# Performance work log

Hardware: AMD Instinct MI355X
Metric: run time of the kernel (lower is better)

## Reference

```python
import jax, jax.numpy as jnp
import numpy as np

N = 32768      # total nodes
E = 262144     # total edges (avg degree 8)
S = 128        # graph segments
B = 16         # batch entries
C = S // B     # segments per batch entry
NF, NC = 90, 36
OP, OD = 120, 64
D0, DX, GIN, GH = 190, 380, 256, 512


def setup_inputs() -> dict:
    key = jax.random.key(0)
    ks = jax.random.split(key, 16)
    rn = lambda k, shape, s=0.02: jax.random.normal(k, shape, jnp.float32) * s
    return {
        "node_features": jax.random.normal(ks[0], (N, NF), jnp.float32),
        "node_config_features": jax.random.normal(ks[1], (N, NC), jnp.float32),
        "emb_table": rn(ks[2], (OP, OD), 1.0),
        "w1": rn(ks[3], (DX, D0)), "b1": jnp.zeros((DX,), jnp.float32),
        "g1": jnp.ones((DX,), jnp.float32), "be1": jnp.zeros((DX,), jnp.float32),
        "w2": rn(ks[4], (GIN, DX)), "b2": jnp.zeros((GIN,), jnp.float32),
        "g2": jnp.ones((GIN,), jnp.float32), "be2": jnp.zeros((GIN,), jnp.float32),
        "wl1": rn(ks[5], (GH, GIN)), "bl1": jnp.zeros((GH,), jnp.float32), "wr1": rn(ks[6], (GH, GIN)),
        "wl2": rn(ks[7], (GH, GH)), "bl2": jnp.zeros((GH,), jnp.float32), "wr2": rn(ks[8], (GH, GH)),
        "wl3": rn(ks[9], (GH, GH)), "bl3": jnp.zeros((GH,), jnp.float32), "wr3": rn(ks[10], (GH, GH)),
        "wc": rn(ks[11], (1, GH)), "bc": jnp.zeros((1,), jnp.float32),
        "node_ops": jax.random.randint(ks[12], (N,), 0, OP),
        "edges": jax.random.randint(ks[13], (2, E), 0, N),
        # cumulative end indices, equal-size segments; batches = segment -> batch entry
        "node_separation": (jnp.arange(S, dtype=jnp.int32) + 1) * (N // S),
        "batches": jnp.repeat(jnp.arange(B, dtype=jnp.int32), C),
    }


def _leaky(x):
    return jnp.where(x >= 0, x, 0.01 * x)


def _graphwise_ln(x, seg_id, counts, gamma, beta):
    # per-graph-segment mean/var over all nodes and features, per-feature affine
    D = x.shape[1]
    s = jax.ops.segment_sum(jnp.sum(x, -1), seg_id, num_segments=S)
    ss = jax.ops.segment_sum(jnp.sum(x * x, -1), seg_id, num_segments=S)
    cnt = counts.astype(x.dtype) * D
    mean = s / cnt
    var = ss / cnt - mean * mean
    inv = jax.lax.rsqrt(var + 1e-5)
    return (x - mean[seg_id, None]) * inv[seg_id, None] * gamma + beta


def _pairnorm(x):
    # PyG PairNorm, scale=1: center over nodes, divide by sqrt(mean row norm^2)
    xc = x - jnp.mean(x, axis=0, keepdims=True)
    denom = 1e-5 + jnp.sqrt(jnp.mean(jnp.sum(xc * xc, -1)))
    return xc / denom


def _sage(x, src, dst, inv_deg, wl, bl, wr):
    # SAGEConv(mean): lin_l(mean_neighbors) + lin_r(x)
    agg = jax.ops.segment_sum(x[src], dst, num_segments=N) * inv_deg[:, None]
    return agg @ wl.T + bl + x @ wr.T


def reference(node_features, node_config_features, emb_table, w1, b1, g1, be1,
              w2, b2, g2, be2, wl1, bl1, wr1, wl2, bl2, wr2, wl3, bl3, wr3,
              wc, bc, node_ops, edges, node_separation, batches):
    seg_id = jnp.searchsorted(node_separation, jnp.arange(N), side="right")
    counts = jnp.diff(node_separation, prepend=0)
    src, dst = edges[0], edges[1]
    deg = jax.ops.segment_sum(jnp.ones((E,), jnp.float32), dst, num_segments=N)
    inv_deg = 1.0 / jnp.maximum(deg, 1.0)

    x = jnp.concatenate([node_features, node_config_features, emb_table[node_ops]], axis=1)
    # node_features_mlp: Linear -> LeakyReLU -> GLN -> Linear -> LeakyReLU -> GLN
    x = _graphwise_ln(_leaky(x @ w1.T + b1), seg_id, counts, g1, be1)
    x = _graphwise_ln(_leaky(x @ w2.T + b2), seg_id, counts, g2, be2)
    # GraphSAGE: 3 layers, PairNorm + ReLU after all but the last
    x = jax.nn.relu(_pairnorm(_sage(x, src, dst, inv_deg, wl1, bl1, wr1)))
    x = jax.nn.relu(_pairnorm(_sage(x, src, dst, inv_deg, wl2, bl2, wr2)))
    x = _sage(x, src, dst, inv_deg, wl3, bl3, wr3)
    # ragged per-segment sum pooling (replaces the python loop) -> [S, GH]
    seg_sums = jax.ops.segment_sum(x, seg_id, num_segments=S)
    # batches = repeat(arange(B), C) and segments are in order -> reshape groups
    agg = seg_sums.reshape(B, C, GH)
    out = agg @ wc.T + bc  # [B, C, 1]
    return jnp.squeeze(out, 2)
```

## Files before the change

### kernel.cpp

```cpp
#include <hip/hip_runtime.h>
#include <hip/hip_bf16.h>

#define NN   32768
#define EE   262144
#define SS   128
#define NF_  90
#define NC_  36
#define OD_  64
#define D0_  190
#define DX_  380
#define GIN_ 256
#define GH_  512

typedef __attribute__((ext_vector_type(8))) short  s8v;
typedef __attribute__((ext_vector_type(4))) float  f4v;

typedef const __attribute__((address_space(1))) void* gas_ptr;
typedef __attribute__((address_space(3))) void*       las_ptr;

__device__ __forceinline__ float bf2f(unsigned short u) {
  return __uint_as_float(((unsigned)u) << 16);
}
__device__ __forceinline__ unsigned short f2bf(float f) {
  unsigned u = __float_as_uint(f);
  u += 0x7FFFu + ((u >> 16) & 1u);
  return (unsigned short)(u >> 16);
}

__global__ void deg_count(const int* __restrict__ dst, int* __restrict__ deg) {
  int e = blockIdx.x * 256 + threadIdx.x;
  if (e < EE) atomicAdd(&deg[dst[e]], 1);
}

__global__ void inv_deg_k(const int* __restrict__ deg, float* __restrict__ inv_deg) {
  int n = blockIdx.x * 256 + threadIdx.x;
  if (n < NN) inv_deg[n] = 1.0f / fmaxf((float)deg[n], 1.0f);
}

__global__ __launch_bounds__(256) void blk_sum_k(const int* __restrict__ deg,
                                                 int* __restrict__ bsum) {
  __shared__ int buf[256];
  int tid = threadIdx.x;
  buf[tid] = deg[blockIdx.x * 256 + tid];
  __syncthreads();
  for (int off = 128; off > 0; off >>= 1) {
    if (tid < off) buf[tid] += buf[tid + off];
    __syncthreads();
  }
  if (tid == 0) bsum[blockIdx.x] = buf[0];
}

__global__ __launch_bounds__(128) void blk_scan_k(const int* __restrict__ bsum,
                                                  int* __restrict__ boff) {
  __shared__ int buf[128];
  int tid = threadIdx.x;
  int v = bsum[tid];
  buf[tid] = v;
  __syncthreads();
  for (int d = 1; d < 128; d <<= 1) {
    int t = (tid >= d) ? buf[tid - d] : 0;
    __syncthreads();
    if (tid >= d) buf[tid] += t;
    __syncthreads();
  }
  boff[tid] = buf[tid] - v;
}

__global__ __launch_bounds__(256) void offsets_k(const int* __restrict__ deg,
                                                 const int* __restrict__ boff,
                                                 int* __restrict__ offsets) {
  __shared__ int buf[256];
  int tid = threadIdx.x;
  int i = blockIdx.x * 256 + tid;
  int v = deg[i];
  buf[tid] = v;
  __syncthreads();
  for (int d = 1; d < 256; d <<= 1) {
    int t = (tid >= d) ? buf[tid - d] : 0;
    __syncthreads();
    if (tid >= d) buf[tid] += t;
    __syncthreads();
  }
  offsets[i] = boff[blockIdx.x] + buf[tid] - v;
  if (i == 0) offsets[NN] = EE;
}

__global__ void bucket_k(const int* __restrict__ src, const int* __restrict__ dst,
                         const int* __restrict__ offsets, int* __restrict__ cursor,
                         int* __restrict__ srcs) {
  int e = blockIdx.x * 256 + threadIdx.x;
  if (e < EE) {
    int d = dst[e];
    int pos = offsets[d] + atomicAdd(&cursor[d], 1);
    srcs[pos] = src[e];
  }
}

#define CW1  73728
#define CW2  172032
#define CWL1 303104
#define CWR1 434176
#define CWL2 696320
#define CWR2 958464
#define CWL3 1220608
#define CWR3 1482752

__global__ void conv_all(const float* __restrict__ w1, const float* __restrict__ w2,
                         const float* __restrict__ wl1, const float* __restrict__ wr1,
                         const float* __restrict__ wl2, const float* __restrict__ wr2,
                         const float* __restrict__ wl3, const float* __restrict__ wr3,
                         unsigned short* __restrict__ w1b, unsigned short* __restrict__ w2b,
                         unsigned short* __restrict__ wl1b, unsigned short* __restrict__ wr1b,
                         unsigned short* __restrict__ wl2b, unsigned short* __restrict__ wr2b,
                         unsigned short* __restrict__ wl3b, unsigned short* __restrict__ wr3b) {
  int idx = blockIdx.x * 256 + threadIdx.x;
  if (idx >= CWR3) return;
  if (idx < CW1) {
    int r = idx / 192, c = idx - r * 192;
    w1b[idx] = f2bf((r < DX_ && c < D0_) ? w1[r * D0_ + c] : 0.0f);
  } else if (idx < CW2) {
    int i = idx - CW1;
    int r = i / 384, c = i - r * 384;
    w2b[i] = f2bf((c < DX_) ? w2[r * DX_ + c] : 0.0f);
  } else if (idx < CWL1) { int i = idx - CW2;  wl1b[i] = f2bf(wl1[i]); }
  else if (idx < CWR1)   { int i = idx - CWL1; wr1b[i] = f2bf(wr1[i]); }
  else if (idx < CWL2)   { int i = idx - CWR1; wl2b[i] = f2bf(wl2[i]); }
  else if (idx < CWR2)   { int i = idx - CWL2; wr2b[i] = f2bf(wr2[i]); }
  else if (idx < CWL3)   { int i = idx - CWR2; wl3b[i] = f2bf(wl3[i]); }
  else                   { int i = idx - CWL3; wr3b[i] = f2bf(wr3[i]); }
}

__global__ void build_x0_bf16(const float* __restrict__ nf, const float* __restrict__ ncf,
                              const float* __restrict__ emb, const int* __restrict__ ops,
                              unsigned short* __restrict__ x0) {
  int idx = blockIdx.x * 256 + threadIdx.x;
  if (idx >= NN * 192) return;
  int n = idx / 192;
  int c = idx - n * 192;
  float v;
  if (c < NF_)            v = nf[n * NF_ + c];
  else if (c < NF_ + NC_) v = ncf[n * NC_ + (c - NF_)];
  else if (c < D0_)       v = emb[ops[n] * OD_ + (c - (NF_ + NC_))];
  else                    v = 0.0f;
  x0[idx] = f2bf(v);
}

__device__ __forceinline__ void stage_tile_async(const unsigned short* __restrict__ G, int ld,
                                                 int base_row, int k0,
                                                 unsigned short* __restrict__ lds, int tid) {
#pragma unroll
  for (int i = 0; i < 2; ++i) {
    int c = tid + i * 256;
    int row = c & 127;
    int off = c >> 7;
    const unsigned short* src = G + (size_t)(base_row + row) * ld + k0 + off * 8;
    unsigned short* dst = lds + off * 1024 + row * 8;
    __builtin_amdgcn_global_load_lds((gas_ptr)(const void*)src, (las_ptr)(void*)dst,
                                     16, 0, 0);
  }
}

__global__ __launch_bounds__(256) void mfma_gemm2(
    const unsigned short* __restrict__ A1, int lda1,
    const unsigned short* __restrict__ B1, int ldb1, int K1,
    const unsigned short* __restrict__ A2, int lda2,
    const unsigned short* __restrict__ B2, int ldb2, int K2,
    const float* __restrict__ bias,
    float* __restrict__ C, int ldc, int Nreal, int mode, int swz,
    float* __restrict__ st0, float* __restrict__ st1,
    const float* __restrict__ wcp, float* __restrict__ outp)
{
  __shared__ unsigned short As[4096];
  __shared__ unsigned short Bs[4096];
  __shared__ float red[256];
  __shared__ float cs[128], css[128];
  int tid = threadIdx.x;
  int lane = tid & 63;
  int w = tid >> 6;
  int wm = (w & 1) * 64;
  int wn = (w >> 1) * 64;
  int bm, bn;
  if (swz) {
    int L = blockIdx.x;
    int xcd = L & 7;
    int s = L >> 3;
    bn = (s & 3) * 128;
    bm = ((s >> 2) * 8 + xcd) * 128;
  } else {
    bm = blockIdx.y * 128;
    bn = blockIdx.x * 128;
  }
  int quad = lane >> 4;
  int r16 = lane & 15;

  f4v acc[4][4] = {};

#pragma unroll 1
  for (int ph = 0; ph < 2; ++ph) {
    const unsigned short* A = ph ? A2 : A1;
    const unsigned short* B = ph ? B2 : B1;
    int lda = ph ? lda2 : lda1;
    int ldb = ph ? ldb2 : ldb1;
    int K = ph ? K2 : K1;
    for (int k0 = 0; k0 < K; k0 += 32) {
      stage_tile_async(A, lda, bm, k0, As, tid);
      stage_tile_async(B, ldb, bn, k0, Bs, tid);
      __syncthreads();
      s8v af[4], bfr[4];
#pragma unroll
      for (int mi = 0; mi < 4; ++mi)
        af[mi] = *(const s8v*)&As[quad * 1024 + (wm + mi * 16 + r16) * 8];
#pragma unroll
      for (int ni = 0; ni < 4; ++ni)
        bfr[ni] = *(const s8v*)&Bs[quad * 1024 + (wn + ni * 16 + r16) * 8];
#pragma unroll
      for (int mi = 0; mi < 4; ++mi)
#pragma unroll
        for (int ni = 0; ni < 4; ++ni)
          acc[mi][ni] = __builtin_amdgcn_mfma_f32_16x16x32_bf16(
              af[mi], bfr[ni], acc[mi][ni], 0, 0, 0);
      __syncthreads();
    }
  }

  int seg = bm >> 8;

  if (mode == 1) {
    float lsum = 0.0f, lssq = 0.0f;
#pragma unroll
    for (int mi = 0; mi < 4; ++mi) {
      int gm = bm + wm + mi * 16 + quad * 4;
#pragma unroll
      for (int ni = 0; ni < 4; ++ni) {
        int gn = bn + wn + ni * 16 + r16;
        if (gn < Nreal) {
          float bv = bias[gn];
#pragma unroll
          for (int r = 0; r < 4; ++r) {
            float v = acc[mi][ni][r] + bv;
            v = (v >= 0.0f) ? v : 0.01f * v;
            C[(size_t)(gm + r) * ldc + gn] = v;
            lsum += v;
            lssq += v * v;
          }
        }
      }
    }
    red[tid] = lsum;
    __syncthreads();
    for (int off = 128; off > 0; off >>= 1) {
      if (tid < off) red[tid] += red[tid + off];
      __syncthreads();
    }
    if (tid == 0) atomicAdd(&st0[seg], red[0]);
    __syncthreads();
    red[tid] = lssq;
    __syncthreads();
    for (int off = 128; off > 0; off >>= 1) {
      if (tid < off) red[tid] += red[tid + off];
      __syncthreads();
    }
    if (tid == 0) atomicAdd(&st1[seg], red[0]);
  } else if (mode == 2) {
    if (tid < 128) { cs[tid] = 0.0f; css[tid] = 0.0f; }
    __syncthreads();
#pragma unroll
    for (int ni = 0; ni < 4; ++ni) {
      int col = wn + ni * 16 + r16;
      int gn = bn + col;
      float bv = bias[gn];
      float psum = 0.0f, pssq = 0.0f;
#pragma unroll
      for (int mi = 0; mi < 4; ++mi) {
        int gm = bm + wm + mi * 16 + quad * 4;
#pragma unroll
        for (int r = 0; r < 4; ++r) {
          float v = acc[mi][ni][r] + bv;
          C[(size_t)(gm + r) * ldc + gn] = v;
          psum += v;
          pssq += v * v;
        }
      }
      atomicAdd(&cs[col], psum);
      atomicAdd(&css[col], pssq);
    }
    __syncthreads();
    if (tid < 128) {
      atomicAdd(&st0[bn + tid], cs[tid]);
      atomicAdd(&st1[bn + tid], css[tid]);
    }
  } else {
    float part = 0.0f;
#pragma unroll
    for (int ni = 0; ni < 4; ++ni) {
      int gn = bn + wn + ni * 16 + r16;
      float bv = bias[gn];
      float wv = wcp[gn];
      float colsum = 0.0f;
#pragma unroll
      for (int mi = 0; mi < 4; ++mi)
#pragma unroll
        for (int r = 0; r < 4; ++r)
          colsum += acc[mi][ni][r] + bv;
      part += colsum * wv;
    }
    red[tid] = part;
    __syncthreads();
    for (int off = 128; off > 0; off >>= 1) {
      if (tid < off) red[tid] += red[tid + off];
      __syncthreads();
    }
    if (tid == 0) atomicAdd(&outp[seg], red[0]);
  }
}

__global__ __launch_bounds__(256) void gln_apply_bf16(
    const float* __restrict__ x, int ld, int D, int Dp,
    const float* __restrict__ seg_sum, const float* __restrict__ seg_ssq,
    const float* __restrict__ g, const float* __restrict__ be,
    unsigned short* __restrict__ out) {
  int r = blockIdx.x;
  int s = r >> 8;
  float cnt = 256.0f * (float)D;
  float m = seg_sum[s] / cnt;
  float var = seg_ssq[s] / cnt - m * m;
  float inv = rsqrtf(var + 1e-5f);
  const float* row = x + (size_t)r * ld;
  unsigned short* orow = out + (size_t)r * Dp;
  for (int c = threadIdx.x; c < Dp; c += 256) {
    float v = (c < D) ? ((row[c] - m) * inv * g[c] + be[c]) : 0.0f;
    orow[c] = f2bf(v);
  }
}

__global__ __launch_bounds__(256) void aggregate4(const unsigned short* __restrict__ x,
                                                  int D4log,
                                                  unsigned short* __restrict__ agg,
                                                  const int* __restrict__ offsets,
                                                  const int* __restrict__ srcs,
                                                  const float* __restrict__ inv_deg) {
  int tid = threadIdx.x;
  int D4 = 1 << D4log;
  int npb = 256 >> D4log;
  int n = blockIdx.x * npb + (tid >> D4log);
  int f4 = tid & (D4 - 1);
  int start = offsets[n], end = offsets[n + 1];
  float wgt = inv_deg[n];
  const uint2* xb = (const uint2*)x;
  float a0 = 0.0f, a1 = 0.0f, a2 = 0.0f, a3 = 0.0f;
  for (int e = start; e < end; ++e) {
    uint2 v = xb[((size_t)srcs[e] << D4log) + f4];
    a0 += bf2f((unsigned short)(v.x & 0xffffu));
    a1 += bf2f((unsigned short)(v.x >> 16));
    a2 += bf2f((unsigned short)(v.y & 0xffffu));
    a3 += bf2f((unsigned short)(v.y >> 16));
  }
  uint2 o;
  o.x = ((unsigned)f2bf(a1 * wgt) << 16) | (unsigned)f2bf(a0 * wgt);
  o.y = ((unsigned)f2bf(a3 * wgt) << 16) | (unsigned)f2bf(a2 * wgt);
  ((uint2*)agg)[((size_t)n << D4log) + f4] = o;
}

__global__ __launch_bounds__(512) void pn_finalize(const float* __restrict__ colsum,
                                                   const float* __restrict__ colssq,
                                                   float* __restrict__ mu,
                                                   float* __restrict__ invd) {
  int f = threadIdx.x;
  float m = colsum[f] / (float)NN;
  mu[f] = m;
  float t = colssq[f] / (float)NN - m * m;
  __shared__ float buf[512];
  buf[f] = t;
  __syncthreads();
  for (int off = 256; off > 0; off >>= 1) {
    if (f < off) buf[f] += buf[f + off];
    __syncthreads();
  }
  if (f == 0) invd[0] = 1.0f / (1e-5f + sqrtf(fmaxf(buf[0], 0.0f)));
}

__global__ __launch_bounds__(128) void pn_apply_v(const float* __restrict__ y,
                                                  const float* __restrict__ mu,
                                                  const float* __restrict__ invd,
                                                  unsigned short* __restrict__ xb) {
  int r = blockIdx.x;
  int f4 = threadIdx.x;
  float id = invd[0];
  float4 v = ((const float4*)(y + (size_t)r * GH_))[f4];
  float4 m = ((const float4*)mu)[f4];
  float v0 = fmaxf((v.x - m.x) * id, 0.0f);
  float v1 = fmaxf((v.y - m.y) * id, 0.0f);
  float v2 = fmaxf((v.z - m.z) * id, 0.0f);
  float v3 = fmaxf((v.w - m.w) * id, 0.0f);
  uint2 o;
  o.x = ((unsigned)f2bf(v1) << 16) | (unsigned)f2bf(v0);
  o.y = ((unsigned)f2bf(v3) << 16) | (unsigned)f2bf(v2);
  ((uint2*)(xb + (size_t)r * GH_))[f4] = o;
}

__global__ void init_out(float* __restrict__ out, const float* __restrict__ bc) {
  int s = threadIdx.x;
  if (s < SS) out[s] = bc[0];
}

extern "C" void kernel_launch(void* const* d_in, const int* in_sizes, int n_in,
                              void* d_out, int out_size, void* d_ws, size_t ws_size,
                              hipStream_t stream) {
  const float* node_features = (const float*)d_in[0];
  const float* node_config   = (const float*)d_in[1];
  const float* emb_table     = (const float*)d_in[2];
  const float* w1  = (const float*)d_in[3];
  const float* b1  = (const float*)d_in[4];
  const float* g1  = (const float*)d_in[5];
  const float* be1 = (const float*)d_in[6];
  const float* w2  = (const float*)d_in[7];
  const float* b2  = (const float*)d_in[8];
  const float* g2  = (const float*)d_in[9];
  const float* be2 = (const float*)d_in[10];
  const float* wl1 = (const float*)d_in[11];
  const float* bl1 = (const float*)d_in[12];
  const float* wr1 = (const float*)d_in[13];
  const float* wl2 = (const float*)d_in[14];
  const float* bl2 = (const float*)d_in[15];
  const float* wr2 = (const float*)d_in[16];
  const float* wl3 = (const float*)d_in[17];
  const float* bl3 = (const float*)d_in[18];
  const float* wr3 = (const float*)d_in[19];
  const float* wc  = (const float*)d_in[20];
  const float* bc  = (const float*)d_in[21];
  const int* node_ops = (const int*)d_in[22];
  const int* edges    = (const int*)d_in[23];
  float* out = (float*)d_out;

  char* ws = (char*)d_ws;
  size_t off = 0;
  auto alloc = [&](size_t bytes) -> void* {
    void* p = ws + off;
    off += (bytes + 255) & ~(size_t)255;
    return p;
  };

  int*   deg_i   = (int*)alloc(NN * 4);
  int*   cursor  = (int*)alloc(NN * 4);
  int*   offsets = (int*)alloc((NN + 1) * 4);
  int*   srcs    = (int*)alloc(EE * 4);
  int*   bsum    = (int*)alloc(SS * 4);
  int*   boff    = (int*)alloc(SS * 4);
  float* inv_deg = (float*)alloc(NN * 4);
  float* seg_sum = (float*)alloc(SS * 4);
  float* seg_ssq = (float*)alloc(SS * 4);
  float* colsum  = (float*)alloc(512 * 4);
  float* colssq  = (float*)alloc(512 * 4);
  float* mu      = (float*)alloc(512 * 4);
  float* invd    = (float*)alloc(256);
  unsigned short* w1b  = (unsigned short*)alloc((size_t)384 * 192 * 2);
  unsigned short* w2b  = (unsigned short*)alloc((size_t)256 * 384 * 2);
  unsigned short* wl1b = (unsigned short*)alloc((size_t)512 * 256 * 2);
  unsigned short* wr1b = (unsigned short*)alloc((size_t)512 * 256 * 2);
  unsigned short* wl2b = (unsigned short*)alloc((size_t)512 * 512 * 2);
  unsigned short* wr2b = (unsigned short*)alloc((size_t)512 * 512 * 2);
  unsigned short* wl3b = (unsigned short*)alloc((size_t)512 * 512 * 2);
  unsigned short* wr3b = (unsigned short*)alloc((size_t)512 * 512 * 2);
  float*          Y    = (float*)alloc((size_t)NN * 512 * 4);
  unsigned short* BF1  = (unsigned short*)alloc((size_t)NN * 512 * 2);
  unsigned short* BF2  = (unsigned short*)alloc((size_t)NN * 512 * 2);
  unsigned short* BF3  = (unsigned short*)alloc((size_t)NN * 512 * 2);

  const int* esrc = edges;
  const int* edst = edges + EE;

  hipMemsetAsync(deg_i, 0, NN * 4, stream);
  hipMemsetAsync(cursor, 0, NN * 4, stream);
  deg_count<<<EE / 256, 256, 0, stream>>>(edst, deg_i);
  blk_sum_k<<<NN / 256, 256, 0, stream>>>(deg_i, bsum);
  blk_scan_k<<<1, 128, 0, stream>>>(bsum, boff);
  offsets_k<<<NN / 256, 256, 0, stream>>>(deg_i, boff, offsets);
  inv_deg_k<<<NN / 256, 256, 0, stream>>>(deg_i, inv_deg);
  bucket_k<<<EE / 256, 256, 0, stream>>>(esrc, edst, offsets, cursor, srcs);

  conv_all<<<(CWR3 + 255) / 256, 256, 0, stream>>>(w1, w2, wl1, wr1, wl2, wr2, wl3, wr3,
                                                   w1b, w2b, wl1b, wr1b, wl2b, wr2b,
                                                   wl3b, wr3b);

  init_out<<<1, SS, 0, stream>>>(out, bc);

  build_x0_bf16<<<(NN * 192 + 255) / 256, 256, 0, stream>>>(node_features, node_config,
                                                            emb_table, node_ops, BF1);
  hipMemsetAsync(seg_sum, 0, 1024, stream);
  {
    dim3 g(384 / 128, NN / 128);
    mfma_gemm2<<<g, 256, 0, stream>>>(BF1, 192, w1b, 192, 192,
                                      nullptr, 0, nullptr, 0, 0,
                                      b1, Y, 384, DX_, 1, 0,
                                      seg_sum, seg_ssq, nullptr, nullptr);
  }
  gln_apply_bf16<<<NN, 256, 0, stream>>>(Y, 384, DX_, 384, seg_sum, seg_ssq, g1, be1, BF2);

  hipMemsetAsync(seg_sum, 0, 1024, stream);
  {
    dim3 g(256 / 128, NN / 128);
    mfma_gemm2<<<g, 256, 0, stream>>>(BF2, 384, w2b, 384, 384,
                                      nullptr, 0, nullptr, 0, 0,
                                      b2, Y, 256, GIN_, 1, 0,
                                      seg_sum, seg_ssq, nullptr, nullptr);
  }
  gln_apply_bf16<<<NN, 256, 0, stream>>>(Y, 256, GIN_, 256, seg_sum, seg_ssq, g2, be2, BF3);

  aggregate4<<<NN / 4, 256, 0, stream>>>(BF3, 6, BF1, offsets, srcs, inv_deg);
  hipMemsetAsync(colsum, 0, 4096, stream);
  mfma_gemm2<<<1024, 256, 0, stream>>>(BF1, 256, wl1b, 256, 256,
                                       BF3, 256, wr1b, 256, 256,
                                       bl1, Y, 512, GH_, 2, 1,
                                       colsum, colssq, nullptr, nullptr);
  pn_finalize<<<1, 512, 0, stream>>>(colsum, colssq, mu, invd);
  pn_apply_v<<<NN, 128, 0, stream>>>(Y, mu, invd, BF2);

  aggregate4<<<NN / 2, 256, 0, stream>>>(BF2, 7, BF1, offsets, srcs, inv_deg);
  hipMemsetAsync(colsum, 0, 4096, stream);
  mfma_gemm2<<<1024, 256, 0, stream>>>(BF1, 512, wl2b, 512, 512,
                                       BF2, 512, wr2b, 512, 512,
                                       bl2, Y, 512, GH_, 2, 1,
                                       colsum, colssq, nullptr, nullptr);
  pn_finalize<<<1, 512, 0, stream>>>(colsum, colssq, mu, invd);
  pn_apply_v<<<NN, 128, 0, stream>>>(Y, mu, invd, BF3);

  aggregate4<<<NN / 2, 256, 0, stream>>>(BF3, 7, BF1, offsets, srcs, inv_deg);
  mfma_gemm2<<<1024, 256, 0, stream>>>(BF1, 512, wl3b, 512, 512,
                                       BF3, 512, wr3b, 512, 512,
                                       bl3, nullptr, 512, GH_, 3, 1,
                                       nullptr, nullptr, wc, out);
}
```

Measured before the change: 663.7 us.

## Fuse pipeline stages into persistent kernels with software grid barriers

Folds weight conversion, input packing, the GEMMs, graph-wise layernorm, aggregation and PairNorm into five kernels. Atomic-counter grid barriers separate the phases, and normalisation statistics are applied straight from the accumulator registers. This removes the fp32 intermediate Y round trip, several small launches and the separate normalise passes. Correctness depends on all 768–1024 blocks being co-resident at occupancy 4 per CU, otherwise the barriers deadlock. The barrier spin also adds synchronisation cost.

```diff
diff --git a/kernel.cpp b/kernel.cpp
--- a/kernel.cpp
+++ b/kernel.cpp
@@ -27,14 +27,22 @@
   return (unsigned short)(u >> 16);
 }
 
+__device__ __forceinline__ void grid_bar(int* bar, int nb) {
+  __syncthreads();
+  if (threadIdx.x == 0) {
+    __threadfence();
+    __hip_atomic_fetch_add(bar, 1, __ATOMIC_RELEASE, __HIP_MEMORY_SCOPE_AGENT);
+    while (__hip_atomic_load(bar, __ATOMIC_RELAXED, __HIP_MEMORY_SCOPE_AGENT) < nb) {
+      __builtin_amdgcn_s_sleep(2);
+    }
+  }
+  __syncthreads();
+  __threadfence();
+}
+
 __global__ void deg_count(const int* __restrict__ dst, int* __restrict__ deg) {
   int e = blockIdx.x * 256 + threadIdx.x;
   if (e < EE) atomicAdd(&deg[dst[e]], 1);
-}
-
-__global__ void inv_deg_k(const int* __restrict__ deg, float* __restrict__ inv_deg) {
-  int n = blockIdx.x * 256 + threadIdx.x;
-  if (n < NN) inv_deg[n] = 1.0f / fmaxf((float)deg[n], 1.0f);
 }
 
 __global__ __launch_bounds__(256) void blk_sum_k(const int* __restrict__ deg,
@@ -68,7 +76,8 @@
 
 __global__ __launch_bounds__(256) void offsets_k(const int* __restrict__ deg,
                                                  const int* __restrict__ boff,
-                                                 int* __restrict__ offsets) {
+                                                 int* __restrict__ offsets,
+                                                 float* __restrict__ inv_deg) {
   __shared__ int buf[256];
   int tid = threadIdx.x;
   int i = blockIdx.x * 256 + tid;
@@ -82,6 +91,7 @@
     __syncthreads();
   }
   offsets[i] = boff[blockIdx.x] + buf[tid] - v;
+  inv_deg[i] = 1.0f / fmaxf((float)v, 1.0f);
   if (i == 0) offsets[NN] = EE;
 }
 
@@ -96,55 +106,6 @@
   }
 }
 
-#define CW1  73728
-#define CW2  172032
-#define CWL1 303104
-#define CWR1 434176
-#define CWL2 696320
-#define CWR2 958464
-#define CWL3 1220608
-#define CWR3 1482752
-
-__global__ void conv_all(const float* __restrict__ w1, const float* __restrict__ w2,
-                         const float* __restrict__ wl1, const float* __restrict__ wr1,
-                         const float* __restrict__ wl2, const float* __restrict__ wr2,
-                         const float* __restrict__ wl3, const float* __restrict__ wr3,
-                         unsigned short* __restrict__ w1b, unsigned short* __restrict__ w2b,
-                         unsigned short* __restrict__ wl1b, unsigned short* __restrict__ wr1b,
-                         unsigned short* __restrict__ wl2b, unsigned short* __restrict__ wr2b,
-                         unsigned short* __restrict__ wl3b, unsigned short* __restrict__ wr3b) {
-  int idx = blockIdx.x * 256 + threadIdx.x;
-  if (idx >= CWR3) return;
-  if (idx < CW1) {
-    int r = idx / 192, c = idx - r * 192;
-    w1b[idx] = f2bf((r < DX_ && c < D0_) ? w1[r * D0_ + c] : 0.0f);
-  } else if (idx < CW2) {
-    int i = idx - CW1;
-    int r = i / 384, c = i - r * 384;
-    w2b[i] = f2bf((c < DX_) ? w2[r * DX_ + c] : 0.0f);
-  } else if (idx < CWL1) { int i = idx - CW2;  wl1b[i] = f2bf(wl1[i]); }
-  else if (idx < CWR1)   { int i = idx - CWL1; wr1b[i] = f2bf(wr1[i]); }
-  else if (idx < CWL2)   { int i = idx - CWR1; wl2b[i] = f2bf(wl2[i]); }
-  else if (idx < CWR2)   { int i = idx - CWL2; wr2b[i] = f2bf(wr2[i]); }
-  else if (idx < CWL3)   { int i = idx - CWR2; wl3b[i] = f2bf(wl3[i]); }
-  else                   { int i = idx - CWL3; wr3b[i] = f2bf(wr3[i]); }
-}
-
-__global__ void build_x0_bf16(const float* __restrict__ nf, const float* __restrict__ ncf,
-                              const float* __restrict__ emb, const int* __restrict__ ops,
-                              unsigned short* __restrict__ x0) {
-  int idx = blockIdx.x * 256 + threadIdx.x;
-  if (idx >= NN * 192) return;
-  int n = idx / 192;
-  int c = idx - n * 192;
-  float v;
-  if (c < NF_)            v = nf[n * NF_ + c];
-  else if (c < NF_ + NC_) v = ncf[n * NC_ + (c - NF_)];
-  else if (c < D0_)       v = emb[ops[n] * OD_ + (c - (NF_ + NC_))];
-  else                    v = 0.0f;
-  x0[idx] = f2bf(v);
-}
-
 __device__ __forceinline__ void stage_tile_async(const unsigned short* __restrict__ G, int ld,
                                                  int base_row, int k0,
                                                  unsigned short* __restrict__ lds, int tid) {
@@ -160,41 +121,20 @@
   }
 }
 
-__global__ __launch_bounds__(256) void mfma_gemm2(
+__device__ __forceinline__ void gemm_core(
     const unsigned short* __restrict__ A1, int lda1,
     const unsigned short* __restrict__ B1, int ldb1, int K1,
     const unsigned short* __restrict__ A2, int lda2,
     const unsigned short* __restrict__ B2, int ldb2, int K2,
-    const float* __restrict__ bias,
-    float* __restrict__ C, int ldc, int Nreal, int mode, int swz,
-    float* __restrict__ st0, float* __restrict__ st1,
-    const float* __restrict__ wcp, float* __restrict__ outp)
+    int bm, int bn, int tid,
+    unsigned short* As, unsigned short* Bs, f4v (&acc)[4][4])
 {
-  __shared__ unsigned short As[4096];
-  __shared__ unsigned short Bs[4096];
-  __shared__ float red[256];
-  __shared__ float cs[128], css[128];
-  int tid = threadIdx.x;
   int lane = tid & 63;
   int w = tid >> 6;
   int wm = (w & 1) * 64;
   int wn = (w >> 1) * 64;
-  int bm, bn;
-  if (swz) {
-    int L = blockIdx.x;
-    int xcd = L & 7;
-    int s = L >> 3;
-    bn = (s & 3) * 128;
-    bm = ((s >> 2) * 8 + xcd) * 128;
-  } else {
-    bm = blockIdx.y * 128;
-    bn = blockIdx.x * 128;
-  }
   int quad = lane >> 4;
   int r16 = lane & 15;
-
-  f4v acc[4][4] = {};
-
 #pragma unroll 1
   for (int ph = 0; ph < 2; ++ph) {
     const unsigned short* A = ph ? A2 : A1;
@@ -222,61 +162,290 @@
       __syncthreads();
     }
   }
+}
+
+#define CW1  73728
+#define CW2  172032
+#define CWL1 303104
+#define CWR1 434176
+#define CWL2 696320
+#define CWR2 958464
+#define CWL3 1220608
+#define CWR3 1482752
+
+__global__ __launch_bounds__(256, 4) void k_mlp1(
+    const float* __restrict__ nf, const float* __restrict__ ncf,
+    const float* __restrict__ emb, const int* __restrict__ ops,
+    const float* __restrict__ w1, const float* __restrict__ w2,
+    const float* __restrict__ wl1, const float* __restrict__ wr1,
+    const float* __restrict__ wl2, const float* __restrict__ wr2,
+    const float* __restrict__ wl3, const float* __restrict__ wr3,
+    unsigned short* __restrict__ w1b, unsigned short* __restrict__ w2b,
+    unsigned short* __restrict__ wl1b, unsigned short* __restrict__ wr1b,
+    unsigned short* __restrict__ wl2b, unsigned short* __restrict__ wr2b,
+    unsigned short* __restrict__ wl3b, unsigned short* __restrict__ wr3b,
+    unsigned short* __restrict__ x0,
+    const float* __restrict__ b1, const float* __restrict__ g1,
+    const float* __restrict__ be1,
+    unsigned short* __restrict__ outbf,
+    float* __restrict__ stat_all, float* __restrict__ outp,
+    const float* __restrict__ bc, int* bar0, int* bar1)
+{
+  __shared__ unsigned short As[4096];
+  __shared__ unsigned short Bs[4096];
+  __shared__ float red[256];
+  int tid = threadIdx.x;
+  int L = blockIdx.x;
+  const int T = 768 * 256;
+  int gidx = L * 256 + tid;
+
+  for (int i = gidx; i < 2560; i += T) stat_all[i] = 0.0f;
+  if (gidx < SS) outp[gidx] = bc[0];
+  for (int i = gidx; i < CWR3; i += T) {
+    if (i < CW1) {
+      int r = i / 192, c = i - r * 192;
+      w1b[i] = f2bf((r < DX_ && c < D0_) ? w1[r * D0_ + c] : 0.0f);
+    } else if (i < CW2) {
+      int j = i - CW1;
+      int r = j / 384, c = j - r * 384;
+      w2b[j] = f2bf((c < DX_) ? w2[r * DX_ + c] : 0.0f);
+    } else if (i < CWL1) { int j = i - CW2;  wl1b[j] = f2bf(wl1[j]); }
+    else if (i < CWR1)   { int j = i - CWL1; wr1b[j] = f2bf(wr1[j]); }
+    else if (i < CWL2)   { int j = i - CWR1; wl2b[j] = f2bf(wl2[j]); }
+    else if (i < CWR2)   { int j = i - CWL2; wr2b[j] = f2bf(wr2[j]); }
+    else if (i < CWL3)   { int j = i - CWR2; wl3b[j] = f2bf(wl3[j]); }
+    else                 { int j = i - CWL3; wr3b[j] = f2bf(wr3[j]); }
+  }
+  for (int i = gidx; i < NN * 192; i += T) {
+    int n = i / 192;
+    int c = i - n * 192;
+    float v;
+    if (c < NF_)            v = nf[n * NF_ + c];
+    else if (c < NF_ + NC_) v = ncf[n * NC_ + (c - NF_)];
+    else if (c < D0_)       v = emb[ops[n] * OD_ + (c - (NF_ + NC_))];
+    else                    v = 0.0f;
+    x0[i] = f2bf(v);
+  }
+  grid_bar(bar0, 768);
+
+  int bn = (L % 3) * 128;
+  int bm = (L / 3) * 128;
+  int lane = tid & 63;
+  int w = tid >> 6;
+  int wm = (w & 1) * 64, wn = (w >> 1) * 64;
+  int quad = lane >> 4, r16 = lane & 15;
+  f4v acc[4][4] = {};
+  gemm_core(x0, 192, w1b, 192, 192, nullptr, 0, nullptr, 0, 0,
+            bm, bn, tid, As, Bs, acc);
 
   int seg = bm >> 8;
-
-  if (mode == 1) {
-    float lsum = 0.0f, lssq = 0.0f;
-#pragma unroll
-    for (int mi = 0; mi < 4; ++mi) {
-      int gm = bm + wm + mi * 16 + quad * 4;
-#pragma unroll
-      for (int ni = 0; ni < 4; ++ni) {
-        int gn = bn + wn + ni * 16 + r16;
-        if (gn < Nreal) {
-          float bv = bias[gn];
-#pragma unroll
-          for (int r = 0; r < 4; ++r) {
-            float v = acc[mi][ni][r] + bv;
-            v = (v >= 0.0f) ? v : 0.01f * v;
-            C[(size_t)(gm + r) * ldc + gn] = v;
-            lsum += v;
-            lssq += v * v;
-          }
+  float lsum = 0.0f, lssq = 0.0f;
+#pragma unroll
+  for (int mi = 0; mi < 4; ++mi) {
+#pragma unroll
+    for (int ni = 0; ni < 4; ++ni) {
+      int gn = bn + wn + ni * 16 + r16;
+      if (gn < DX_) {
+        float bv = b1[gn];
+#pragma unroll
+        for (int r = 0; r < 4; ++r) {
+          float v = acc[mi][ni][r] + bv;
+          v = (v >= 0.0f) ? v : 0.01f * v;
+          acc[mi][ni][r] = v;
+          lsum += v;
+          lssq += v * v;
         }
       }
     }
-    red[tid] = lsum;
-    __syncthreads();
-    for (int off = 128; off > 0; off >>= 1) {
-      if (tid < off) red[tid] += red[tid + off];
-      __syncthreads();
-    }
-    if (tid == 0) atomicAdd(&st0[seg], red[0]);
-    __syncthreads();
-    red[tid] = lssq;
-    __syncthreads();
-    for (int off = 128; off > 0; off >>= 1) {
-      if (tid < off) red[tid] += red[tid + off];
-      __syncthreads();
-    }
-    if (tid == 0) atomicAdd(&st1[seg], red[0]);
-  } else if (mode == 2) {
+  }
+  red[tid] = lsum;
+  __syncthreads();
+  for (int off = 128; off > 0; off >>= 1) {
+    if (tid < off) red[tid] += red[tid + off];
+    __syncthreads();
+  }
+  if (tid == 0) atomicAdd(&stat_all[seg], red[0]);
+  __syncthreads();
+  red[tid] = lssq;
+  __syncthreads();
+  for (int off = 128; off > 0; off >>= 1) {
+    if (tid < off) red[tid] += red[tid + off];
+    __syncthreads();
+  }
+  if (tid == 0) atomicAdd(&stat_all[128 + seg], red[0]);
+
+  grid_bar(bar1, 768);
+
+  float cnt = 256.0f * (float)DX_;
+  float m = stat_all[seg] / cnt;
+  float var = stat_all[128 + seg] / cnt - m * m;
+  float inv = rsqrtf(var + 1e-5f);
+#pragma unroll
+  for (int mi = 0; mi < 4; ++mi) {
+    int gm = bm + wm + mi * 16 + quad * 4;
+#pragma unroll
+    for (int ni = 0; ni < 4; ++ni) {
+      int gn = bn + wn + ni * 16 + r16;
+      float gg = (gn < DX_) ? g1[gn] : 0.0f;
+      float bb = (gn < DX_) ? be1[gn] : 0.0f;
+#pragma unroll
+      for (int r = 0; r < 4; ++r) {
+        float vv = (gn < DX_) ? ((acc[mi][ni][r] - m) * inv * gg + bb) : 0.0f;
+        outbf[(size_t)(gm + r) * 384 + gn] = f2bf(vv);
+      }
+    }
+  }
+}
+
+__global__ __launch_bounds__(256, 4) void k_mlp2(
+    const unsigned short* __restrict__ A,
+    const unsigned short* __restrict__ wb,
+    const float* __restrict__ b2, const float* __restrict__ g2,
+    const float* __restrict__ be2,
+    unsigned short* __restrict__ outbf,
+    float* __restrict__ stat_all, int* bar0)
+{
+  __shared__ unsigned short As[4096];
+  __shared__ unsigned short Bs[4096];
+  __shared__ float red[256];
+  int tid = threadIdx.x;
+  int L = blockIdx.x;
+  int bn = (L % 2) * 128;
+  int bm = (L / 2) * 128;
+  int lane = tid & 63;
+  int w = tid >> 6;
+  int wm = (w & 1) * 64, wn = (w >> 1) * 64;
+  int quad = lane >> 4, r16 = lane & 15;
+  f4v acc[4][4] = {};
+  gemm_core(A, 384, wb, 384, 384, nullptr, 0, nullptr, 0, 0,
+            bm, bn, tid, As, Bs, acc);
+
+  int seg = bm >> 8;
+  float lsum = 0.0f, lssq = 0.0f;
+#pragma unroll
+  for (int mi = 0; mi < 4; ++mi) {
+#pragma unroll
+    for (int ni = 0; ni < 4; ++ni) {
+      int gn = bn + wn + ni * 16 + r16;
+      float bv = b2[gn];
+#pragma unroll
+      for (int r = 0; r < 4; ++r) {
+        float v = acc[mi][ni][r] + bv;
+        v = (v >= 0.0f) ? v : 0.01f * v;
+        acc[mi][ni][r] = v;
+        lsum += v;
+        lssq += v * v;
+      }
+    }
+  }
+  red[tid] = lsum;
+  __syncthreads();
+  for (int off = 128; off > 0; off >>= 1) {
+    if (tid < off) red[tid] += red[tid + off];
+    __syncthreads();
+  }
+  if (tid == 0) atomicAdd(&stat_all[256 + seg], red[0]);
+  __syncthreads();
+  red[tid] = lssq;
+  __syncthreads();
+  for (int off = 128; off > 0; off >>= 1) {
+    if (tid < off) red[tid] += red[tid + off];
+    __syncthreads();
+  }
+  if (tid == 0) atomicAdd(&stat_all[384 + seg], red[0]);
+
+  grid_bar(bar0, 512);
+
+  float cnt = 256.0f * (float)GIN_;
+  float m = stat_all[256 + seg] / cnt;
+  float var = stat_all[384 + seg] / cnt - m * m;
+  float inv = rsqrtf(var + 1e-5f);
+#pragma unroll
+  for (int mi = 0; mi < 4; ++mi) {
+    int gm = bm + wm + mi * 16 + quad * 4;
+#pragma unroll
+    for (int ni = 0; ni < 4; ++ni) {
+      int gn = bn + wn + ni * 16 + r16;
+      float gg = g2[gn], bb = be2[gn];
+#pragma unroll
+      for (int r = 0; r < 4; ++r) {
+        float vv = (acc[mi][ni][r] - m) * inv * gg + bb;
+        outbf[(size_t)(gm + r) * 256 + gn] = f2bf(vv);
+      }
+    }
+  }
+}
+
+__global__ __launch_bounds__(256, 4) void k_sage(
+    const unsigned short* __restrict__ x, int D4log,
+    unsigned short* __restrict__ aggb,
+    const int* __restrict__ offsets, const int* __restrict__ srcs,
+    const float* __restrict__ inv_deg,
+    const unsigned short* __restrict__ wl, const unsigned short* __restrict__ wr,
+    const float* __restrict__ bias, int mode,
+    float* __restrict__ cs0, float* __restrict__ cs1,
+    unsigned short* __restrict__ outx,
+    const float* __restrict__ wc, float* __restrict__ outp,
+    int* bar_a, int* bar_b)
+{
+  __shared__ unsigned short As[4096];
+  __shared__ unsigned short Bs[4096];
+  __shared__ float red[256];
+  __shared__ float cs[128], css[128];
+  int tid = threadIdx.x;
+  int L = blockIdx.x;
+  int D = 4 << D4log;
+
+  {
+    int D4 = 1 << D4log;
+    int npb = 256 >> D4log;
+    int f4 = tid & (D4 - 1);
+    const uint2* xb = (const uint2*)x;
+    for (int it = 0; it < 32 / npb * npb; it += npb) {
+      int n = L * 32 + it + (tid >> D4log);
+      int start = offsets[n], end = offsets[n + 1];
+      float wgt = inv_deg[n];
+      float a0 = 0.0f, a1 = 0.0f, a2 = 0.0f, a3 = 0.0f;
+      for (int e = start; e < end; ++e) {
+        uint2 v = xb[((size_t)srcs[e] << D4log) + f4];
+        a0 += bf2f((unsigned short)(v.x & 0xffffu));
+        a1 += bf2f((unsigned short)(v.x >> 16));
+        a2 += bf2f((unsigned short)(v.y & 0xffffu));
+        a3 += bf2f((unsigned short)(v.y >> 16));
+      }
+      uint2 o;
+      o.x = ((unsigned)f2bf(a1 * wgt) << 16) | (unsigned)f2bf(a0 * wgt);
+      o.y = ((unsigned)f2bf(a3 * wgt) << 16) | (unsigned)f2bf(a2 * wgt);
+      ((uint2*)aggb)[((size_t)n << D4log) + f4] = o;
+    }
+  }
+  grid_bar(bar_a, 1024);
+
+  int xcd = L & 7;
+  int s = L >> 3;
+  int bn = (s & 3) * 128;
+  int bm = ((s >> 2) * 8 + xcd) * 128;
+  int lane = tid & 63;
+  int w = tid >> 6;
+  int wm = (w & 1) * 64, wn = (w >> 1) * 64;
+  int quad = lane >> 4, r16 = lane & 15;
+  f4v acc[4][4] = {};
+  gemm_core(aggb, D, wl, D, D, x, D, wr, D, D, bm, bn, tid, As, Bs, acc);
+
+  if (mode == 2) {
     if (tid < 128) { cs[tid] = 0.0f; css[tid] = 0.0f; }
     __syncthreads();
 #pragma unroll
     for (int ni = 0; ni < 4; ++ni) {
       int col = wn + ni * 16 + r16;
-      int gn = bn + col;
-      float bv = bias[gn];
+      float bv = bias[bn + col];
       float psum = 0.0f, pssq = 0.0f;
 #pragma unroll
       for (int mi = 0; mi < 4; ++mi) {
-        int gm = bm + wm + mi * 16 + quad * 4;
 #pragma unroll
         for (int r = 0; r < 4; ++r) {
           float v = acc[mi][ni][r] + bv;
-          C[(size_t)(gm + r) * ldc + gn] = v;
+          acc[mi][ni][r] = v;
           psum += v;
           pssq += v * v;
         }
@@ -286,16 +455,47 @@
     }
     __syncthreads();
     if (tid < 128) {
-      atomicAdd(&st0[bn + tid], cs[tid]);
-      atomicAdd(&st1[bn + tid], css[tid]);
+      atomicAdd(&cs0[bn + tid], cs[tid]);
+      atomicAdd(&cs1[bn + tid], css[tid]);
+    }
+    grid_bar(bar_b, 1024);
+
+    const float rN = 1.0f / (float)NN;
+    float t = 0.0f;
+    for (int c = tid; c < 512; c += 256) {
+      float m = cs0[c] * rN;
+      t += cs1[c] * rN - m * m;
+    }
+    red[tid] = t;
+    __syncthreads();
+    for (int off = 128; off > 0; off >>= 1) {
+      if (tid < off) red[tid] += red[tid + off];
+      __syncthreads();
+    }
+    float invd = 1.0f / (1e-5f + sqrtf(fmaxf(red[0], 0.0f)));
+    __syncthreads();
+#pragma unroll
+    for (int mi = 0; mi < 4; ++mi) {
+      int gm = bm + wm + mi * 16 + quad * 4;
+#pragma unroll
+      for (int ni = 0; ni < 4; ++ni) {
+        int gn = bn + wn + ni * 16 + r16;
+        float mu = cs0[gn] * rN;
+#pragma unroll
+        for (int r = 0; r < 4; ++r) {
+          float vv = fmaxf((acc[mi][ni][r] - mu) * invd, 0.0f);
+          outx[(size_t)(gm + r) * GH_ + gn] = f2bf(vv);
+        }
+      }
     }
   } else {
+    int seg = bm >> 8;
     float part = 0.0f;
 #pragma unroll
     for (int ni = 0; ni < 4; ++ni) {
       int gn = bn + wn + ni * 16 + r16;
       float bv = bias[gn];
-      float wv = wcp[gn];
+      float wv = wc[gn];
       float colsum = 0.0f;
 #pragma unroll
       for (int mi = 0; mi < 4; ++mi)
@@ -312,95 +512,6 @@
     }
     if (tid == 0) atomicAdd(&outp[seg], red[0]);
   }
-}
-
-__global__ __launch_bounds__(256) void gln_apply_bf16(
-    const float* __restrict__ x, int ld, int D, int Dp,
-    const float* __restrict__ seg_sum, const float* __restrict__ seg_ssq,
-    const float* __restrict__ g, const float* __restrict__ be,
-    unsigned short* __restrict__ out) {
-  int r = blockIdx.x;
-  int s = r >> 8;
-  float cnt = 256.0f * (float)D;
-  float m = seg_sum[s] / cnt;
-  float var = seg_ssq[s] / cnt - m * m;
-  float inv = rsqrtf(var + 1e-5f);
-  const float* row = x + (size_t)r * ld;
-  unsigned short* orow = out + (size_t)r * Dp;
-  for (int c = threadIdx.x; c < Dp; c += 256) {
-    float v = (c < D) ? ((row[c] - m) * inv * g[c] + be[c]) : 0.0f;
-    orow[c] = f2bf(v);
-  }
-}
-
-__global__ __launch_bounds__(256) void aggregate4(const unsigned short* __restrict__ x,
-                                                  int D4log,
-                                                  unsigned short* __restrict__ agg,
-                                                  const int* __restrict__ offsets,
-                                                  const int* __restrict__ srcs,
-                                                  const float* __restrict__ inv_deg) {
-  int tid = threadIdx.x;
-  int D4 = 1 << D4log;
-  int npb = 256 >> D4log;
-  int n = blockIdx.x * npb + (tid >> D4log);
-  int f4 = tid & (D4 - 1);
-  int start = offsets[n], end = offsets[n + 1];
-  float wgt = inv_deg[n];
-  const uint2* xb = (const uint2*)x;
-  float a0 = 0.0f, a1 = 0.0f, a2 = 0.0f, a3 = 0.0f;
-  for (int e = start; e < end; ++e) {
-    uint2 v = xb[((size_t)srcs[e] << D4log) + f4];
-    a0 += bf2f((unsigned short)(v.x & 0xffffu));
-    a1 += bf2f((unsigned short)(v.x >> 16));
-    a2 += bf2f((unsigned short)(v.y & 0xffffu));
-    a3 += bf2f((unsigned short)(v.y >> 16));
-  }
-  uint2 o;
-  o.x = ((unsigned)f2bf(a1 * wgt) << 16) | (unsigned)f2bf(a0 * wgt);
-  o.y = ((unsigned)f2bf(a3 * wgt) << 16) | (unsigned)f2bf(a2 * wgt);
-  ((uint2*)agg)[((size_t)n << D4log) + f4] = o;
-}
-
-__global__ __launch_bounds__(512) void pn_finalize(const float* __restrict__ colsum,
-                                                   const float* __restrict__ colssq,
-                                                   float* __restrict__ mu,
-                                                   float* __restrict__ invd) {
-  int f = threadIdx.x;
-  float m = colsum[f] / (float)NN;
-  mu[f] = m;
-  float t = colssq[f] / (float)NN - m * m;
-  __shared__ float buf[512];
-  buf[f] = t;
-  __syncthreads();
-  for (int off = 256; off > 0; off >>= 1) {
-    if (f < off) buf[f] += buf[f + off];
-    __syncthreads();
-  }
-  if (f == 0) invd[0] = 1.0f / (1e-5f + sqrtf(fmaxf(buf[0], 0.0f)));
-}
-
-__global__ __launch_bounds__(128) void pn_apply_v(const float* __restrict__ y,
-                                                  const float* __restrict__ mu,
-                                                  const float* __restrict__ invd,
-                                                  unsigned short* __restrict__ xb) {
-  int r = blockIdx.x;
-  int f4 = threadIdx.x;
-  float id = invd[0];
-  float4 v = ((const float4*)(y + (size_t)r * GH_))[f4];
-  float4 m = ((const float4*)mu)[f4];
-  float v0 = fmaxf((v.x - m.x) * id, 0.0f);
-  float v1 = fmaxf((v.y - m.y) * id, 0.0f);
-  float v2 = fmaxf((v.z - m.z) * id, 0.0f);
-  float v3 = fmaxf((v.w - m.w) * id, 0.0f);
-  uint2 o;
-  o.x = ((unsigned)f2bf(v1) << 16) | (unsigned)f2bf(v0);
-  o.y = ((unsigned)f2bf(v3) << 16) | (unsigned)f2bf(v2);
-  ((uint2*)(xb + (size_t)r * GH_))[f4] = o;
-}
-
-__global__ void init_out(float* __restrict__ out, const float* __restrict__ bc) {
-  int s = threadIdx.x;
-  if (s < SS) out[s] = bc[0];
 }
 
 extern "C" void kernel_launch(void* const* d_in, const int* in_sizes, int n_in,
@@ -442,17 +553,13 @@
 
   int*   deg_i   = (int*)alloc(NN * 4);
   int*   cursor  = (int*)alloc(NN * 4);
+  int*   bars    = (int*)alloc(16 * 4);
   int*   offsets = (int*)alloc((NN + 1) * 4);
   int*   srcs    = (int*)alloc(EE * 4);
   int*   bsum    = (int*)alloc(SS * 4);
   int*   boff    = (int*)alloc(SS * 4);
   float* inv_deg = (float*)alloc(NN * 4);
-  float* seg_sum = (float*)alloc(SS * 4);
-  float* seg_ssq = (float*)alloc(SS * 4);
-  float* colsum  = (float*)alloc(512 * 4);
-  float* colssq  = (float*)alloc(512 * 4);
-  float* mu      = (float*)alloc(512 * 4);
-  float* invd    = (float*)alloc(256);
+  float* stat_all= (float*)alloc(2560 * 4);
   unsigned short* w1b  = (unsigned short*)alloc((size_t)384 * 192 * 2);
   unsigned short* w2b  = (unsigned short*)alloc((size_t)256 * 384 * 2);
   unsigned short* wl1b = (unsigned short*)alloc((size_t)512 * 256 * 2);
@@ -461,7 +568,6 @@
   unsigned short* wr2b = (unsigned short*)alloc((size_t)512 * 512 * 2);
   unsigned short* wl3b = (unsigned short*)alloc((size_t)512 * 512 * 2);
   unsigned short* wr3b = (unsigned short*)alloc((size_t)512 * 512 * 2);
-  float*          Y    = (float*)alloc((size_t)NN * 512 * 4);
   unsigned short* BF1  = (unsigned short*)alloc((size_t)NN * 512 * 2);
   unsigned short* BF2  = (unsigned short*)alloc((size_t)NN * 512 * 2);
   unsigned short* BF3  = (unsigned short*)alloc((size_t)NN * 512 * 2);
@@ -469,64 +575,35 @@
   const int* esrc = edges;
   const int* edst = edges + EE;
 
-  hipMemsetAsync(deg_i, 0, NN * 4, stream);
-  hipMemsetAsync(cursor, 0, NN * 4, stream);
+  hipMemsetAsync(deg_i, 0, (size_t)NN * 4 * 2 + 256, stream);
+
   deg_count<<<EE / 256, 256, 0, stream>>>(edst, deg_i);
   blk_sum_k<<<NN / 256, 256, 0, stream>>>(deg_i, bsum);
   blk_scan_k<<<1, 128, 0, stream>>>(bsum, boff);
-  offsets_k<<<NN / 256, 256, 0, stream>>>(deg_i, boff, offsets);
-  inv_deg_k<<<NN / 256, 256, 0, stream>>>(deg_i, inv_deg);
+  offsets_k<<<NN / 256, 256, 0, stream>>>(deg_i, boff, offsets, inv_deg);
   bucket_k<<<EE / 256, 256, 0, stream>>>(esrc, edst, offsets, cursor, srcs);
 
-  conv_all<<<(CWR3 + 255) / 256, 256, 0, stream>>>(w1, w2, wl1, wr1, wl2, wr2, wl3, wr3,
-                                                   w1b, w2b, wl1b, wr1b, wl2b, wr2b,
-                                                   wl3b, wr3b);
-
-  init_out<<<1, SS, 0, stream>>>(out, bc);
-
-  build_x0_bf16<<<(NN * 192 + 255) / 256, 256, 0, stream>>>(node_features, node_config,
-                                                            emb_table, node_ops, BF1);
-  hipMemsetAsync(seg_sum, 0, 1024, stream);
-  {
-    dim3 g(384 / 128, NN / 128);
-    mfma_gemm2<<<g, 256, 0, stream>>>(BF1, 192, w1b, 192, 192,
-                                      nullptr, 0, nullptr, 0, 0,
-                                      b1, Y, 384, DX_, 1, 0,
-                                      seg_sum, seg_ssq, nullptr, nullptr);
-  }
-  gln_apply_bf16<<<NN, 256, 0, stream>>>(Y, 384, DX_, 384, seg_sum, seg_ssq, g1, be1, BF2);
-
-  hipMemsetAsync(seg_sum, 0, 1024, stream);
-  {
-    dim3 g(256 / 128, NN / 128);
-    mfma_gemm2<<<g, 256, 0, stream>>>(BF2, 384, w2b, 384, 384,
-                                      nullptr, 0, nullptr, 0, 0,
-                                      b2, Y, 256, GIN_, 1, 0,
-                                      seg_sum, seg_ssq, nullptr, nullptr);
-  }
-  gln_apply_bf16<<<NN, 256, 0, stream>>>(Y, 256, GIN_, 256, seg_sum, seg_ssq, g2, be2, BF3);
-
-  aggregate4<<<NN / 4, 256, 0, stream>>>(BF3, 6, BF1, offsets, srcs, inv_deg);
-  hipMemsetAsync(colsum, 0, 4096, stream);
-  mfma_gemm2<<<1024, 256, 0, stream>>>(BF1, 256, wl1b, 256, 256,
-                                       BF3, 256, wr1b, 256, 256,
-                                       bl1, Y, 512, GH_, 2, 1,
-                                       colsum, colssq, nullptr, nullptr);
-  pn_finalize<<<1, 512, 0, stream>>>(colsum, colssq, mu, invd);
-  pn_apply_v<<<NN, 128, 0, stream>>>(Y, mu, invd, BF2);
-
-  aggregate4<<<NN / 2, 256, 0, stream>>>(BF2, 7, BF1, offsets, srcs, inv_deg);
-  hipMemsetAsync(colsum, 0, 4096, stream);
-  mfma_gemm2<<<1024, 256, 0, stream>>>(BF1, 512, wl2b, 512, 512,
-                                       BF2, 512, wr2b, 512, 512,
-                                       bl2, Y, 512, GH_, 2, 1,
-                                       colsum, colssq, nullptr, nullptr);
-  pn_finalize<<<1, 512, 0, stream>>>(colsum, colssq, mu, invd);
-  pn_apply_v<<<NN, 128, 0, stream>>>(Y, mu, invd, BF3);
-
-  aggregate4<<<NN / 2, 256, 0, stream>>>(BF3, 7, BF1, offsets, srcs, inv_deg);
-  mfma_gemm2<<<1024, 256, 0, stream>>>(BF1, 512, wl3b, 512, 512,
-                                       BF3, 512, wr3b, 512, 512,
-                                       bl3, nullptr, 512, GH_, 3, 1,
-                                       nullptr, nullptr, wc, out);
-}
+  k_mlp1<<<768, 256, 0, stream>>>(node_features, node_config, emb_table, node_ops,
+                                  w1, w2, wl1, wr1, wl2, wr2, wl3, wr3,
+                                  w1b, w2b, wl1b, wr1b, wl2b, wr2b, wl3b, wr3b,
+                                  BF1, b1, g1, be1, BF2,
+                                  stat_all, out, bc, &bars[0], &bars[1]);
+
+  k_mlp2<<<512, 256, 0, stream>>>(BF2, w2b, b2, g2, be2, BF3,
+                                  stat_all, &bars[2]);
+
+  k_sage<<<1024, 256, 0, stream>>>(BF3, 6, BF1, offsets, srcs, inv_deg,
+                                   wl1b, wr1b, bl1, 2,
+                                   stat_all + 512, stat_all + 1024, BF2,
+                                   nullptr, nullptr, &bars[3], &bars[4]);
+
+  k_sage<<<1024, 256, 0, stream>>>(BF2, 7, BF1, offsets, srcs, inv_deg,
+                                   wl2b, wr2b, bl2, 2,
+                                   stat_all + 1536, stat_all + 2048, BF3,
+                                   nullptr, nullptr, &bars[5], &bars[6]);
+
+  k_sage<<<1024, 256, 0, stream>>>(BF3, 7, BF1, offsets, srcs, inv_deg,
+                                   wl3b, wr3b, bl3, 3,
+                                   nullptr, nullptr, nullptr,
+                                   wc, out, &bars[7], &bars[8]);
+}
```

Result: slower. 1.903 ms (+186.7%).
